# Performance work log

Measured on AMD Instinct MI355X. Metric: run time of the kernel, lower is better.

The kernel has to match this reference:

```python
import jax, jax.numpy as jnp
import numpy as np

N, E, IN_C, OUT_C, HEADS = 50000, 800000, 256, 256, 4
C = OUT_C // HEADS  # per-head channels = 64
BN_EPS = 1e-5


def setup_inputs() -> dict:
    key = jax.random.key(0)
    ks = jax.random.split(key, 16)
    inp = {
        'x': jax.random.normal(ks[0], (N, IN_C), dtype=jnp.float32),
        'edge_index': jax.random.randint(ks[1], (2, E), 0, N, dtype=jnp.int64),
        'edge_attr': jax.random.uniform(ks[2], (E, 1), dtype=jnp.float32),
        'spatial_coords': jax.random.normal(ks[3], (N, 2), dtype=jnp.float32),
        # GATConv params
        'W_gat': jax.random.normal(ks[4], (IN_C, HEADS * C), dtype=jnp.float32) * 0.05,
        'att_src': jax.random.normal(ks[5], (HEADS, C), dtype=jnp.float32) * 0.05,
        'att_dst': jax.random.normal(ks[6], (HEADS, C), dtype=jnp.float32) * 0.05,
        'bias_gat': jnp.zeros((HEADS * C,), dtype=jnp.float32),
        # spatial_attention MLP (computed but unused by the original forward)
        'w1': jax.random.normal(ks[7], (1, 64), dtype=jnp.float32) * 0.05,
        'b1': jnp.zeros((64,), dtype=jnp.float32),
        'w2': jax.random.normal(ks[8], (64, HEADS), dtype=jnp.float32) * 0.05,
        'b2': jnp.zeros((HEADS,), dtype=jnp.float32),
        # feature_transform: Linear + BatchNorm1d (eval stats) + ReLU (+Dropout=identity)
        'w_ft': jax.random.normal(ks[9], (IN_C, OUT_C), dtype=jnp.float32) * 0.05,
        'b_ft': jnp.zeros((OUT_C,), dtype=jnp.float32),
        'bn_gamma': jnp.ones((OUT_C,), dtype=jnp.float32),
        'bn_beta': jnp.zeros((OUT_C,), dtype=jnp.float32),
        'bn_mean': jax.random.normal(ks[10], (OUT_C,), dtype=jnp.float32) * 0.01,
        'bn_var': jax.random.uniform(ks[11], (OUT_C,), dtype=jnp.float32, minval=0.5, maxval=1.5),
    }
    return inp


def _forward(x, edge_index, edge_attr, W_gat, att_src, att_dst, bias_gat,
             w1, b1, w2, b2, w_ft, b_ft, bn_gamma, bn_beta, bn_mean, bn_var):
    n = x.shape[0]
    # add self-loops (PyG GATConv default)
    loop = jnp.arange(n, dtype=edge_index.dtype)
    src = jnp.concatenate([edge_index[0], loop])
    dst = jnp.concatenate([edge_index[1], loop])

    # linear transform: [N, heads, C]
    h = (x @ W_gat).reshape(n, HEADS, C)
    a_src = jnp.einsum('nhc,hc->nh', h, att_src)  # [N, H]
    a_dst = jnp.einsum('nhc,hc->nh', h, att_dst)  # [N, H]

    # per-edge attention logits, LeakyReLU(0.2)
    alpha = jax.nn.leaky_relu(a_src[src] + a_dst[dst], negative_slope=0.2)  # [Etot, H]
    # segment softmax over incoming edges of each destination node
    amax = jax.ops.segment_max(alpha, dst, num_segments=n)
    alpha = jnp.exp(alpha - amax[dst])
    denom = jax.ops.segment_sum(alpha, dst, num_segments=n)
    alpha = alpha / (denom[dst] + 1e-16)

    # weighted message aggregation
    msg = h[src] * alpha[:, :, None]                        # [Etot, H, C]
    agg = jax.ops.segment_sum(msg, dst, num_segments=n)     # [N, H, C]
    gat_out = agg.reshape(n, HEADS * C) + bias_gat

    # spatial attention weights (computed but UNUSED, matching original)
    spatial_weights = jax.nn.sigmoid(jax.nn.relu(edge_attr @ w1 + b1) @ w2 + b2)
    del spatial_weights

    # feature_transform (BatchNorm in eval mode, Dropout identity)
    y = x @ w_ft + b_ft
    y = (y - bn_mean) * jax.lax.rsqrt(bn_var + BN_EPS) * bn_gamma + bn_beta
    transformed = jax.nn.relu(y)

    return gat_out + transformed


def reference(x, edge_index, edge_attr, spatial_coords, W_gat, att_src, att_dst,
              bias_gat, w1, b1, w2, b2, w_ft, b_ft, bn_gamma, bn_beta, bn_mean, bn_var):
    # spatial_coords is accepted but unused by the original module's forward
    return _forward(x, edge_index, edge_attr, W_gat, att_src, att_dst, bias_gat,
                    w1, b1, w2, b2, w_ft, b_ft, bn_gamma, bn_beta, bn_mean, bn_var)
```

## Files before the change

### kernel.cpp

```cpp
#include <hip/hip_runtime.h>
#include <math.h>

typedef __attribute__((ext_vector_type(4))) float  f32x4;
typedef __attribute__((ext_vector_type(8))) short  short8;
typedef __attribute__((ext_vector_type(4))) unsigned short usx4;
typedef __attribute__((ext_vector_type(8))) unsigned short usx8;

__device__ __forceinline__ float bf2f(unsigned short u) {
    union { unsigned int i; float f; } c; c.i = ((unsigned int)u) << 16; return c.f;
}
__device__ __forceinline__ unsigned short f2bf(float f) {
    union { float f; unsigned int i; } c; c.f = f;
    unsigned int x = c.i;
    unsigned int r = (x + 0x7FFFu + ((x >> 16) & 1u)) >> 16;
    return (unsigned short)r;
}

__global__ __launch_bounds__(256) void k_convert_x(const float* __restrict__ x,
                                                   unsigned short* __restrict__ xb,
                                                   long total8) {
    long i = (long)blockIdx.x * blockDim.x + threadIdx.x;
    if (i >= total8) return;
    const f32x4* p = (const f32x4*)x;
    f32x4 v0 = p[2 * i], v1 = p[2 * i + 1];
    usx8 o;
    o[0] = f2bf(v0[0]); o[1] = f2bf(v0[1]); o[2] = f2bf(v0[2]); o[3] = f2bf(v0[3]);
    o[4] = f2bf(v1[0]); o[5] = f2bf(v1[1]); o[6] = f2bf(v1[2]); o[7] = f2bf(v1[3]);
    ((usx8*)xb)[i] = o;
}

__global__ __launch_bounds__(256) void k_convert_w(const float* __restrict__ Wg,
                                                   const float* __restrict__ Wf,
                                                   unsigned short* __restrict__ wbt) {
    int idx = blockIdx.x * blockDim.x + threadIdx.x;
    if (idx >= 512 * 256) return;
    int c = idx >> 8;
    int k = idx & 255;
    float v = (c < 256) ? Wg[k * 256 + c] : Wf[k * 256 + (c - 256)];
    wbt[idx] = f2bf(v);
}

#define BM 128
#define BN 128

__global__ __launch_bounds__(256, 4) void k_gemm_fast(
    const unsigned short* __restrict__ xb,
    const unsigned short* __restrict__ wbt,
    unsigned short* __restrict__ hb,
    unsigned short* __restrict__ tb,
    float* __restrict__ out,
    const float* __restrict__ att_s, const float* __restrict__ att_d,
    float* __restrict__ a_src, float* __restrict__ a_dst,
    const float* __restrict__ b_ft, const float* __restrict__ bn_g,
    const float* __restrict__ bn_b, const float* __restrict__ bn_m,
    const float* __restrict__ bn_v, int M) {
    __shared__ unsigned short As[128 * 64];
    __shared__ unsigned short Bs[128 * 64];
    const int t = threadIdx.x;
    const int w = t >> 6, l = t & 63;
    const int wr = w >> 1, wc = w & 1;
    const int bm0 = blockIdx.y * BM;
    const int bn0 = blockIdx.x * BN;
    const int kg = l >> 4;
    const int lm = l & 15;

    const int srow = l >> 3;
    const int scol = ((l & 7) ^ srow) << 3;

    f32x4 acc[4][4] = {};

    for (int kk = 0; kk < 4; kk++) {
        const int k0 = kk * 64;
        __syncthreads();
#pragma unroll
        for (int j = 0; j < 4; j++) {
            int r = ((w * 4 + j) << 3) + srow;
            int ga = bm0 + r; if (ga >= M) ga = M - 1;
            __builtin_amdgcn_global_load_lds(
                (const __attribute__((address_space(1))) unsigned int*)
                    (xb + (long)ga * 256 + k0 + scol),
                (__attribute__((address_space(3))) unsigned int*)
                    (As + ((w * 4 + j) << 9)),
                16, 0, 0);
            __builtin_amdgcn_global_load_lds(
                (const __attribute__((address_space(1))) unsigned int*)
                    (wbt + (long)(bn0 + r) * 256 + k0 + scol),
                (__attribute__((address_space(3))) unsigned int*)
                    (Bs + ((w * 4 + j) << 9)),
                16, 0, 0);
        }
        __syncthreads();
#pragma unroll
        for (int ks = 0; ks < 2; ks++) {
            const int cb = (ks * 64 + kg * 16) ^ ((lm & 7) << 4);
            short8 afr[4], bfr[4];
#pragma unroll
            for (int mi = 0; mi < 4; mi++) {
                int row = wr * 64 + mi * 16 + lm;
                afr[mi] = *(const short8*)((const char*)As + row * 128 + cb);
            }
#pragma unroll
            for (int nj = 0; nj < 4; nj++) {
                int row = wc * 64 + nj * 16 + lm;
                bfr[nj] = *(const short8*)((const char*)Bs + row * 128 + cb);
            }
#pragma unroll
            for (int mi = 0; mi < 4; mi++)
#pragma unroll
                for (int nj = 0; nj < 4; nj++)
                    acc[mi][nj] = __builtin_amdgcn_mfma_f32_16x16x32_bf16(
                        afr[mi], bfr[nj], acc[mi][nj], 0, 0, 0);
        }
    }

    const bool isH = (bn0 < 256);
#pragma unroll
    for (int mi = 0; mi < 4; mi++) {
#pragma unroll
        for (int nj = 0; nj < 4; nj++) {
            int col = bn0 + wc * 64 + nj * 16 + lm;
            f32x4 a = acc[mi][nj];
            int rowbase = bm0 + wr * 64 + mi * 16 + kg * 4;
            if (isH) {
#pragma unroll
                for (int r = 0; r < 4; r++) {
                    int row = rowbase + r;
                    if (row < M) hb[(long)row * 256 + col] = f2bf(a[r]);
                }
            } else {
                int c2 = col - 256;
                float bft = b_ft[c2], mu = bn_m[c2];
                float iv = rsqrtf(bn_v[c2] + 1e-5f);
                float g = bn_g[c2], bt = bn_b[c2];
#pragma unroll
                for (int r = 0; r < 4; r++) {
                    int row = rowbase + r;
                    if (row < M) {
                        float v = (a[r] + bft - mu) * iv * g + bt;
                        v = v > 0.f ? v : 0.f;
                        if (tb) tb[(long)row * 256 + c2] = f2bf(v);
                        else    out[(long)row * 256 + c2] = v;
                    }
                }
            }
        }
    }

    if (isH) {
        const int head = (bn0 >> 6) + wc;
        float as_c[4], ad_c[4];
#pragma unroll
        for (int nj = 0; nj < 4; nj++) {
            as_c[nj] = att_s[head * 64 + nj * 16 + lm];
            ad_c[nj] = att_d[head * 64 + nj * 16 + lm];
        }
#pragma unroll
        for (int mi = 0; mi < 4; mi++) {
#pragma unroll
            for (int r = 0; r < 4; r++) {
                float s1 = 0.f, s2 = 0.f;
#pragma unroll
                for (int nj = 0; nj < 4; nj++) {
                    s1 = fmaf(acc[mi][nj][r], as_c[nj], s1);
                    s2 = fmaf(acc[mi][nj][r], ad_c[nj], s2);
                }
#pragma unroll
                for (int o = 1; o < 16; o <<= 1) {
                    s1 += __shfl_xor(s1, o);
                    s2 += __shfl_xor(s2, o);
                }
                int row = bm0 + wr * 64 + mi * 16 + kg * 4 + r;
                if (lm == 0 && row < M) {
                    a_src[(long)row * 4 + head] = s1;
                    a_dst[(long)row * 4 + head] = s2;
                }
            }
        }
    }
}

#define BK 32
__global__ __launch_bounds__(256) void k_gemm(
    const float* __restrict__ x, const unsigned short* __restrict__ wbt,
    unsigned short* __restrict__ hb, unsigned short* __restrict__ tb,
    float* __restrict__ out,
    const float* __restrict__ att_s, const float* __restrict__ att_d,
    float* __restrict__ a_src, float* __restrict__ a_dst,
    const float* __restrict__ b_ft, const float* __restrict__ bn_g,
    const float* __restrict__ bn_b, const float* __restrict__ bn_m,
    const float* __restrict__ bn_v, int M) {
    __shared__ unsigned short As[BM][BK + 8];
    __shared__ unsigned short Bs[BN][BK + 8];
    const int t = threadIdx.x;
    const int w = t >> 6, lane = t & 63;
    const int wr = w >> 1, wc = w & 1;
    const int bm0 = blockIdx.y * BM;
    const int bn0 = blockIdx.x * BN;
    const int kg = lane >> 4;
    const int lm = lane & 15;
    f32x4 acc[4][4] = {};
    for (int k0 = 0; k0 < 256; k0 += BK) {
        f32x4 a0[2], a1[2];
        usx8 bv[2];
#pragma unroll
        for (int s = 0; s < 2; s++) {
            int seg = t + s * 256;
            int row = seg >> 2;
            int off = (seg & 3) * 8;
            int grow = bm0 + row; if (grow >= M) grow = M - 1;
            const float* ap = x + (long)grow * 256 + k0 + off;
            a0[s] = *(const f32x4*)ap;
            a1[s] = *(const f32x4*)(ap + 4);
            bv[s] = *(const usx8*)(wbt + (long)(bn0 + row) * 256 + k0 + off);
        }
        __syncthreads();
#pragma unroll
        for (int s = 0; s < 2; s++) {
            int seg = t + s * 256;
            int row = seg >> 2;
            int off = (seg & 3) * 8;
            usx8 av;
            av[0] = f2bf(a0[s][0]); av[1] = f2bf(a0[s][1]);
            av[2] = f2bf(a0[s][2]); av[3] = f2bf(a0[s][3]);
            av[4] = f2bf(a1[s][0]); av[5] = f2bf(a1[s][1]);
            av[6] = f2bf(a1[s][2]); av[7] = f2bf(a1[s][3]);
            *(usx8*)&As[row][off] = av;
            *(usx8*)&Bs[row][off] = bv[s];
        }
        __syncthreads();
        short8 afr[4], bfr[4];
#pragma unroll
        for (int mi = 0; mi < 4; mi++)
            afr[mi] = *(const short8*)&As[wr * 64 + mi * 16 + lm][kg * 8];
#pragma unroll
        for (int nj = 0; nj < 4; nj++)
            bfr[nj] = *(const short8*)&Bs[wc * 64 + nj * 16 + lm][kg * 8];
#pragma unroll
        for (int mi = 0; mi < 4; mi++)
#pragma unroll
            for (int nj = 0; nj < 4; nj++)
                acc[mi][nj] = __builtin_amdgcn_mfma_f32_16x16x32_bf16(
                    afr[mi], bfr[nj], acc[mi][nj], 0, 0, 0);
        __syncthreads();
    }
    const bool isH = (bn0 < 256);
#pragma unroll
    for (int mi = 0; mi < 4; mi++) {
#pragma unroll
        for (int nj = 0; nj < 4; nj++) {
            int col = bn0 + wc * 64 + nj * 16 + lm;
            f32x4 a = acc[mi][nj];
            int rowbase = bm0 + wr * 64 + mi * 16 + kg * 4;
            if (isH) {
#pragma unroll
                for (int r = 0; r < 4; r++) {
                    int row = rowbase + r;
                    if (row < M) hb[(long)row * 256 + col] = f2bf(a[r]);
                }
            } else {
                int c2 = col - 256;
                float bft = b_ft[c2], mu = bn_m[c2];
                float iv = rsqrtf(bn_v[c2] + 1e-5f);
                float g = bn_g[c2], bt = bn_b[c2];
#pragma unroll
                for (int r = 0; r < 4; r++) {
                    int row = rowbase + r;
                    if (row < M) {
                        float v = (a[r] + bft - mu) * iv * g + bt;
                        v = v > 0.f ? v : 0.f;
                        if (tb) tb[(long)row * 256 + c2] = f2bf(v);
                        else    out[(long)row * 256 + c2] = v;
                    }
                }
            }
        }
    }
    if (isH) {
        const int head = (bn0 >> 6) + wc;
        float as_c[4], ad_c[4];
#pragma unroll
        for (int nj = 0; nj < 4; nj++) {
            as_c[nj] = att_s[head * 64 + nj * 16 + lm];
            ad_c[nj] = att_d[head * 64 + nj * 16 + lm];
        }
#pragma unroll
        for (int mi = 0; mi < 4; mi++) {
#pragma unroll
            for (int r = 0; r < 4; r++) {
                float s1 = 0.f, s2 = 0.f;
#pragma unroll
                for (int nj = 0; nj < 4; nj++) {
                    s1 = fmaf(acc[mi][nj][r], as_c[nj], s1);
                    s2 = fmaf(acc[mi][nj][r], ad_c[nj], s2);
                }
#pragma unroll
                for (int o = 1; o < 16; o <<= 1) {
                    s1 += __shfl_xor(s1, o);
                    s2 += __shfl_xor(s2, o);
                }
                int row = bm0 + wr * 64 + mi * 16 + kg * 4 + r;
                if (lm == 0 && row < M) {
                    a_src[(long)row * 4 + head] = s1;
                    a_dst[(long)row * 4 + head] = s2;
                }
            }
        }
    }
}

__global__ void k_count(const int* __restrict__ ei, int* __restrict__ deg, int E) {
    int i = blockIdx.x * blockDim.x + threadIdx.x;
    if (i < E) atomicAdd(&deg[ei[E + i]], 1);
}
__global__ __launch_bounds__(256) void k_scan1(const int* __restrict__ deg,
                                               int* __restrict__ offs,
                                               int* __restrict__ bsum, int n) {
    __shared__ int tmp[256];
    int b = blockIdx.x, t = threadIdx.x;
    int base = b * 1024;
    int v[4];
#pragma unroll
    for (int j = 0; j < 4; j++) {
        int i = base + t * 4 + j;
        v[j] = (i < n) ? (deg[i] + 1) : 0;
    }
    int local = v[0] + v[1] + v[2] + v[3];
    tmp[t] = local;
    __syncthreads();
    for (int off = 1; off < 256; off <<= 1) {
        int xv = (t >= off) ? tmp[t - off] : 0;
        __syncthreads();
        tmp[t] += xv;
        __syncthreads();
    }
    int run = tmp[t] - local;
    if (t == 255) bsum[b] = tmp[255];
#pragma unroll
    for (int j = 0; j < 4; j++) {
        int i = base + t * 4 + j;
        if (i < n) offs[i] = run;
        run += v[j];
    }
}
__global__ void k_scan2(int* bsum, int nb) {
    if (threadIdx.x == 0 && blockIdx.x == 0) {
        int acc = 0;
        for (int i = 0; i < nb; i++) { int x = bsum[i]; bsum[i] = acc; acc += x; }
    }
}
__global__ void k_scan3(int* __restrict__ offs, const int* __restrict__ bsum,
                        int* __restrict__ srcs, int n) {
    int i = blockIdx.x * blockDim.x + threadIdx.x;
    if (i < n) {
        int o = offs[i] + bsum[i >> 10];
        offs[i] = o;
        srcs[o] = i;
    }
}
__global__ void k_scatter(const int* __restrict__ ei, const int* __restrict__ offs,
                          int* __restrict__ cursor, int* __restrict__ srcs, int E) {
    int i = blockIdx.x * blockDim.x + threadIdx.x;
    if (i >= E) return;
    int d = ei[E + i];
    int pos = atomicAdd(&cursor[d], 1);
    srcs[offs[d] + 1 + pos] = ei[i];
}

__global__ __launch_bounds__(256, 4) void k_agg(
    const int* __restrict__ offs, const int* __restrict__ srcs,
    const unsigned short* __restrict__ hb,
    const float* __restrict__ a_src, const float* __restrict__ a_dst,
    const float* __restrict__ bias_gat, const unsigned short* __restrict__ tb,
    float* __restrict__ out, int N, int E) {
    const int n = (blockIdx.x * 256 + threadIdx.x) >> 6;
    const int l = threadIdx.x & 63;
    if (n >= N) return;
    const int head = l >> 4;
    const int sub = l & 15;
    const int beg = offs[n];
    const int end = (n + 1 < N) ? offs[n + 1] : (E + N);
    const uint2* hp = (const uint2*)hb + l;

    const float ad = a_dst[(long)n * 4 + head];
    f32x4 acc = {};
    float den = 0.f;

    for (int base = beg; base < end; base += 16) {
        const int len = min(16, end - base);
        int sv = 0;
        float wsel = 0.f;
        if (base + sub < end) {
            sv = srcs[base + sub];
            float lv = a_src[(long)sv * 4 + head] + ad;
            lv = fmaxf(lv, 0.2f * lv);
            wsel = __expf(lv);
        }

        if (len == 16) {
            int s[16];
#pragma unroll
            for (int i = 0; i < 16; ++i) s[i] = __shfl(sv, i);
            uint2 hv[16];
#pragma unroll
            for (int i = 0; i < 16; ++i) hv[i] = hp[s[i] << 6];
            __builtin_amdgcn_sched_barrier(0);
            float wg[16];
#pragma unroll
            for (int i = 0; i < 16; ++i) wg[i] = __shfl(wsel, (l & 48) + i);
#pragma unroll
            for (int i = 0; i < 16; ++i) {
                den += wg[i];
                acc[0] = fmaf(wg[i], __uint_as_float(hv[i].x << 16), acc[0]);
                acc[1] = fmaf(wg[i], __uint_as_float(hv[i].x & 0xFFFF0000u), acc[1]);
                acc[2] = fmaf(wg[i], __uint_as_float(hv[i].y << 16), acc[2]);
                acc[3] = fmaf(wg[i], __uint_as_float(hv[i].y & 0xFFFF0000u), acc[3]);
            }
        } else {
            for (int i = 0; i < len; ++i) {
                int src = __shfl(sv, i);
                float wgt = __shfl(wsel, (l & 48) + i);
                uint2 hv = hp[src << 6];
                den += wgt;
                acc[0] = fmaf(wgt, __uint_as_float(hv.x << 16), acc[0]);
                acc[1] = fmaf(wgt, __uint_as_float(hv.x & 0xFFFF0000u), acc[1]);
                acc[2] = fmaf(wgt, __uint_as_float(hv.y << 16), acc[2]);
                acc[3] = fmaf(wgt, __uint_as_float(hv.y & 0xFFFF0000u), acc[3]);
            }
        }
    }

    const float inv = 1.f / (den + 1e-16f);
    const float4 bv = ((const float4*)bias_gat)[l];
    float4 trf;
    const long rowoff = ((long)n << 8) + l * 4;
    if (tb) {
        uint2 tv = ((const uint2*)(tb + ((long)n << 8)))[l];
        trf.x = __uint_as_float(tv.x << 16);
        trf.y = __uint_as_float(tv.x & 0xFFFF0000u);
        trf.z = __uint_as_float(tv.y << 16);
        trf.w = __uint_as_float(tv.y & 0xFFFF0000u);
    } else {
        trf = *(const float4*)(out + rowoff);
    }
    float4 r;
    r.x = acc[0] * inv + bv.x + trf.x;
    r.y = acc[1] * inv + bv.y + trf.y;
    r.z = acc[2] * inv + bv.z + trf.z;
    r.w = acc[3] * inv + bv.w + trf.w;
    *(float4*)(out + rowoff) = r;
}

extern "C" void kernel_launch(void* const* d_in, const int* in_sizes, int n_in,
                              void* d_out, int out_size, void* d_ws, size_t ws_size,
                              hipStream_t stream) {
    const float* x        = (const float*)d_in[0];
    const int*   ei       = (const int*)d_in[1];
    const float* W_gat    = (const float*)d_in[4];
    const float* att_src  = (const float*)d_in[5];
    const float* att_dst  = (const float*)d_in[6];
    const float* bias_gat = (const float*)d_in[7];
    const float* w_ft     = (const float*)d_in[12];
    const float* b_ft     = (const float*)d_in[13];
    const float* bn_g     = (const float*)d_in[14];
    const float* bn_b     = (const float*)d_in[15];
    const float* bn_m     = (const float*)d_in[16];
    const float* bn_v     = (const float*)d_in[17];
    float* out = (float*)d_out;

    const int N = in_sizes[0] / 256;
    const int E = in_sizes[1] / 2;
    const int ETOT = E + N;

    char* p = (char*)d_ws;
    char* pend = p + ws_size;
    auto alloc = [&](size_t bytes) {
        void* r = (void*)p;
        p += (bytes + 255) & ~(size_t)255;
        return r;
    };
    unsigned short* wbt  = (unsigned short*)alloc((size_t)512 * 256 * 2);
    unsigned short* hb   = (unsigned short*)alloc((size_t)N * 256 * 2);
    float* a_src = (float*)alloc((size_t)N * 4 * 4);
    float* a_dst = (float*)alloc((size_t)N * 4 * 4);
    char* z0 = p;
    int* deg    = (int*)alloc((size_t)N * 4);
    int* cursor = (int*)alloc((size_t)N * 4);
    char* z1 = p;
    int* offs   = (int*)alloc((size_t)(N + 1) * 4);
    int* bsum   = (int*)alloc((size_t)256 * 4);
    int* srcs   = (int*)alloc((size_t)ETOT * 4);
    unsigned short* xb = (unsigned short*)alloc((size_t)N * 256 * 2);
    if (p > pend) xb = nullptr;
    unsigned short* tb = (unsigned short*)alloc((size_t)N * 256 * 2);
    if (p > pend) tb = nullptr;

    k_convert_w<<<(512 * 256 + 255) / 256, 256, 0, stream>>>(W_gat, w_ft, wbt);

    dim3 gg(4, (N + BM - 1) / BM);
    if (xb) {
        long total8 = (long)N * 256 / 8;
        k_convert_x<<<(int)((total8 + 255) / 256), 256, 0, stream>>>(x, xb, total8);
        k_gemm_fast<<<gg, 256, 0, stream>>>(xb, wbt, hb, tb, out, att_src, att_dst,
                                            a_src, a_dst, b_ft, bn_g, bn_b, bn_m, bn_v, N);
    } else {
        k_gemm<<<gg, 256, 0, stream>>>(x, wbt, hb, tb, out, att_src, att_dst,
                                       a_src, a_dst, b_ft, bn_g, bn_b, bn_m, bn_v, N);
    }

    hipMemsetAsync(z0, 0, (size_t)(z1 - z0), stream);
    k_count<<<(E + 255) / 256, 256, 0, stream>>>(ei, deg, E);
    int nb = (N + 1023) / 1024;
    k_scan1<<<nb, 256, 0, stream>>>(deg, offs, bsum, N);
    k_scan2<<<1, 64, 0, stream>>>(bsum, nb);
    k_scan3<<<(N + 255) / 256, 256, 0, stream>>>(offs, bsum, srcs, N);
    k_scatter<<<(E + 255) / 256, 256, 0, stream>>>(ei, offs, cursor, srcs, E);

    k_agg<<<(N * 64 + 255) / 256, 256, 0, stream>>>(offs, srcs, hb, a_src, a_dst,
                                                    bias_gat, tb, out, N, E);
}
```

Measured before the change: 235.5 us.

## Merge prep launches, fold block-sum scan into scan3, use inline-asm gathers in agg

Folds the memset, weight conversion and x conversion into one k_prep launch, and removes the single-thread k_scan2 by having each scan3 thread sum the preceding block totals itself (at most 49 reads). This cuts kernel launches and a serial tiny kernel from the pipeline. In k_agg the 16 neighbour row gathers are issued as inline-asm global loads interleaved with the shuffles, followed by an explicit vmcnt(0) wait, to overlap the weight shuffles with memory latency. It also widens the gather index to 64-bit. The inline asm stops the compiler from scheduling those loads itself.

```diff
diff --git a/kernel.cpp b/kernel.cpp
--- a/kernel.cpp
+++ b/kernel.cpp
@@ -3,12 +3,8 @@
 
 typedef __attribute__((ext_vector_type(4))) float  f32x4;
 typedef __attribute__((ext_vector_type(8))) short  short8;
-typedef __attribute__((ext_vector_type(4))) unsigned short usx4;
 typedef __attribute__((ext_vector_type(8))) unsigned short usx8;
 
-__device__ __forceinline__ float bf2f(unsigned short u) {
-    union { unsigned int i; float f; } c; c.i = ((unsigned int)u) << 16; return c.f;
-}
 __device__ __forceinline__ unsigned short f2bf(float f) {
     union { float f; unsigned int i; } c; c.f = f;
     unsigned int x = c.i;
@@ -16,28 +12,36 @@
     return (unsigned short)r;
 }
 
-__global__ __launch_bounds__(256) void k_convert_x(const float* __restrict__ x,
-                                                   unsigned short* __restrict__ xb,
-                                                   long total8) {
-    long i = (long)blockIdx.x * blockDim.x + threadIdx.x;
-    if (i >= total8) return;
+__global__ __launch_bounds__(256) void k_prep(
+    int* __restrict__ zr, int zn,
+    const float* __restrict__ Wg, const float* __restrict__ Wf,
+    unsigned short* __restrict__ wbt,
+    const float* __restrict__ x, unsigned short* __restrict__ xb,
+    long total8, int nz) {
+    int b = blockIdx.x;
+    if (b < nz) {
+        int i = b * 256 + threadIdx.x;
+        if (i < zn) zr[i] = 0;
+        return;
+    }
+    b -= nz;
+    if (b < 512) {
+        int idx = b * 256 + threadIdx.x;
+        int c = idx >> 8;
+        int k = idx & 255;
+        float v = (c < 256) ? Wg[k * 256 + c] : Wf[k * 256 + (c - 256)];
+        wbt[idx] = f2bf(v);
+        return;
+    }
+    b -= 512;
+    long i = (long)b * 256 + threadIdx.x;
+    if (i >= total8 || !xb) return;
     const f32x4* p = (const f32x4*)x;
     f32x4 v0 = p[2 * i], v1 = p[2 * i + 1];
     usx8 o;
     o[0] = f2bf(v0[0]); o[1] = f2bf(v0[1]); o[2] = f2bf(v0[2]); o[3] = f2bf(v0[3]);
     o[4] = f2bf(v1[0]); o[5] = f2bf(v1[1]); o[6] = f2bf(v1[2]); o[7] = f2bf(v1[3]);
     ((usx8*)xb)[i] = o;
-}
-
-__global__ __launch_bounds__(256) void k_convert_w(const float* __restrict__ Wg,
-                                                   const float* __restrict__ Wf,
-                                                   unsigned short* __restrict__ wbt) {
-    int idx = blockIdx.x * blockDim.x + threadIdx.x;
-    if (idx >= 512 * 256) return;
-    int c = idx >> 8;
-    int k = idx & 255;
-    float v = (c < 256) ? Wg[k * 256 + c] : Wf[k * 256 + (c - 256)];
-    wbt[idx] = f2bf(v);
 }
 
 #define BM 128
@@ -342,20 +346,16 @@
         run += v[j];
     }
 }
-__global__ void k_scan2(int* bsum, int nb) {
-    if (threadIdx.x == 0 && blockIdx.x == 0) {
-        int acc = 0;
-        for (int i = 0; i < nb; i++) { int x = bsum[i]; bsum[i] = acc; acc += x; }
-    }
-}
-__global__ void k_scan3(int* __restrict__ offs, const int* __restrict__ bsum,
-                        int* __restrict__ srcs, int n) {
+__global__ void k_scan3f(int* __restrict__ offs, const int* __restrict__ bsum,
+                         int* __restrict__ srcs, int n) {
     int i = blockIdx.x * blockDim.x + threadIdx.x;
-    if (i < n) {
-        int o = offs[i] + bsum[i >> 10];
-        offs[i] = o;
-        srcs[o] = i;
-    }
+    if (i >= n) return;
+    int nbi = i >> 10;
+    int s = 0;
+    for (int j = 0; j < nbi; j++) s += bsum[j];
+    int o = offs[i] + s;
+    offs[i] = o;
+    srcs[o] = i;
 }
 __global__ void k_scatter(const int* __restrict__ ei, const int* __restrict__ offs,
                           int* __restrict__ cursor, int* __restrict__ srcs, int E) {
@@ -397,16 +397,19 @@
         }
 
         if (len == 16) {
-            int s[16];
-#pragma unroll
-            for (int i = 0; i < 16; ++i) s[i] = __shfl(sv, i);
             uint2 hv[16];
 #pragma unroll
-            for (int i = 0; i < 16; ++i) hv[i] = hp[s[i] << 6];
+            for (int i = 0; i < 16; ++i) {
+                int src = __shfl(sv, i);
+                const uint2* ap = hp + ((long)src << 6);
+                asm volatile("global_load_dwordx2 %0, %1, off"
+                             : "=v"(hv[i]) : "v"(ap));
+            }
+            float wg[16];
+#pragma unroll
+            for (int i = 0; i < 16; ++i) wg[i] = __shfl(wsel, (l & 48) + i);
+            asm volatile("s_waitcnt vmcnt(0)" ::: "memory");
             __builtin_amdgcn_sched_barrier(0);
-            float wg[16];
-#pragma unroll
-            for (int i = 0; i < 16; ++i) wg[i] = __shfl(wsel, (l & 48) + i);
 #pragma unroll
             for (int i = 0; i < 16; ++i) {
                 den += wg[i];
@@ -419,7 +422,7 @@
             for (int i = 0; i < len; ++i) {
                 int src = __shfl(sv, i);
                 float wgt = __shfl(wsel, (l & 48) + i);
-                uint2 hv = hp[src << 6];
+                uint2 hv = hp[(long)src << 6];
                 den += wgt;
                 acc[0] = fmaf(wgt, __uint_as_float(hv.x << 16), acc[0]);
                 acc[1] = fmaf(wgt, __uint_as_float(hv.x & 0xFFFF0000u), acc[1]);
@@ -494,12 +497,15 @@
     unsigned short* tb = (unsigned short*)alloc((size_t)N * 256 * 2);
     if (p > pend) tb = nullptr;
 
-    k_convert_w<<<(512 * 256 + 255) / 256, 256, 0, stream>>>(W_gat, w_ft, wbt);
+    const int zn = (int)((z1 - z0) / 4);
+    const int nz = (zn + 255) / 256;
+    const long total8 = (long)N * 256 / 8;
+    const int nx = xb ? (int)((total8 + 255) / 256) : 0;
+    k_prep<<<nz + 512 + nx, 256, 0, stream>>>((int*)z0, zn, W_gat, w_ft, wbt,
+                                              x, xb, total8, nz);
 
     dim3 gg(4, (N + BM - 1) / BM);
     if (xb) {
-        long total8 = (long)N * 256 / 8;
-        k_convert_x<<<(int)((total8 + 255) / 256), 256, 0, stream>>>(x, xb, total8);
         k_gemm_fast<<<gg, 256, 0, stream>>>(xb, wbt, hb, tb, out, att_src, att_dst,
                                             a_src, a_dst, b_ft, bn_g, bn_b, bn_m, bn_v, N);
     } else {
@@ -507,12 +513,10 @@
                                        a_src, a_dst, b_ft, bn_g, bn_b, bn_m, bn_v, N);
     }
 
-    hipMemsetAsync(z0, 0, (size_t)(z1 - z0), stream);
     k_count<<<(E + 255) / 256, 256, 0, stream>>>(ei, deg, E);
     int nb = (N + 1023) / 1024;
     k_scan1<<<nb, 256, 0, stream>>>(deg, offs, bsum, N);
-    k_scan2<<<1, 64, 0, stream>>>(bsum, nb);
-    k_scan3<<<(N + 255) / 256, 256, 0, stream>>>(offs, bsum, srcs, N);
+    k_scan3f<<<(N + 255) / 256, 256, 0, stream>>>(offs, bsum, srcs, N);
     k_scatter<<<(E + 255) / 256, 256, 0, stream>>>(ei, offs, cursor, srcs, E);
 
     k_agg<<<(N * 64 + 255) / 256, 256, 0, stream>>>(offs, srcs, hb, a_src, a_dst,
```

After: 224.8 us. 1.05x faster.
